# Kernel optimization log

Hardware: AMD Instinct MI355X
Metric: run time of the kernel (lower is better)

## Reference

```python
import jax, jax.numpy as jnp
import numpy as np

N, F, H, Z = 80, 64, 256, 128
OFF = N * (N - 1) // 2  # 3160
E = 800
MPM_ITERS = 50


def _gcn(x, src, dst, W, b, n):
    # PyG GCNConv: add self-loops, symmetric normalization D^-1/2 (A+I) D^-1/2, then +bias
    h = x @ W
    ones = jnp.ones(src.shape[0], dtype=h.dtype)
    deg = jax.ops.segment_sum(ones, dst, num_segments=n)
    dinv = jax.lax.rsqrt(jnp.maximum(deg, 1e-12))
    norm = dinv[src] * dinv[dst]
    out = jax.ops.segment_sum(h[src] * norm[:, None], dst, num_segments=n)
    return out + b


def _bn(h, g, b):
    # BatchNorm1d, training mode (biased batch stats), eps=1e-5
    m = h.mean(0)
    v = ((h - m) ** 2).mean(0)
    return g * (h - m) * jax.lax.rsqrt(v + 1e-5) + b


def setup_inputs() -> dict:
    key = jax.random.key(0)
    ks = jax.random.split(key, 32)
    rn = lambda k, s, sc=0.05: (jax.random.normal(k, s, dtype=jnp.float32) * sc)
    inp = {
        'x': jax.random.normal(ks[0], (N, F), dtype=jnp.float32),
        'edge_index': jax.random.randint(ks[1], (2, E), 0, N, dtype=jnp.int32),
        'adj': jax.random.randint(ks[2], (N, N), 0, 2, dtype=jnp.int32),
        'eps': jax.random.normal(ks[3], (1, Z), dtype=jnp.float32),
        'W1': rn(ks[4], (F, H)), 'b1': jnp.zeros((H,), jnp.float32),
        'g1': jnp.ones((H,), jnp.float32), 'bt1': jnp.zeros((H,), jnp.float32),
        'W2': rn(ks[5], (H, H)), 'b2': jnp.zeros((H,), jnp.float32),
        'g2': jnp.ones((H,), jnp.float32), 'bt2': jnp.zeros((H,), jnp.float32),
        'Wmu': rn(ks[6], (H, Z)), 'bmu': jnp.zeros((Z,), jnp.float32),
        'Wlv': rn(ks[7], (H, Z)), 'blv': jnp.zeros((Z,), jnp.float32),
        'We1': rn(ks[8], (Z, H)), 'be1': jnp.zeros((H,), jnp.float32),
        'We2': rn(ks[9], (H, OFF)), 'be2': jnp.zeros((OFF,), jnp.float32),
        'Wn1': rn(ks[10], (Z, H)), 'bn1': jnp.zeros((H,), jnp.float32),
        'Wn2': rn(ks[11], (H, N)), 'bn2': jnp.zeros((N,), jnp.float32),
    }
    return inp


def reference(x, edge_index, adj, eps, W1, b1, g1, bt1, W2, b2, g2, bt2,
              Wmu, bmu, Wlv, blv, We1, be1, We2, be2, Wn1, bn1, Wn2, bn2):
    n = N
    # ---- encoder: GCN -> BN -> ReLU (x2), mean pool over real nodes ----
    sl = jnp.arange(n, dtype=edge_index.dtype)
    src = jnp.concatenate([edge_index[0], sl])
    dst = jnp.concatenate([edge_index[1], sl])
    h = jax.nn.relu(_bn(_gcn(x, src, dst, W1, b1, n), g1, bt1))
    h = jax.nn.relu(_bn(_gcn(h, src, dst, W2, b2, n), g2, bt2))
    g_vec = h.sum(0, keepdims=True) / n  # [1,H], R_int == n
    mu = g_vec @ Wmu + bmu
    logvar = jnp.clip(g_vec @ Wlv + blv, -4.0, 4.0)
    z = mu + eps * jnp.exp(0.5 * logvar)  # reparam
    # ---- decoder ----
    vec_logits = (jax.nn.relu(z @ We1 + be1) @ We2 + be2)[0]   # [OFF]
    node_logits = (jax.nn.relu(z @ Wn1 + bn1) @ Wn2 + bn2)[0]  # [N]
    iu, ju = np.triu_indices(n, k=1)
    A_hat = jnp.zeros((n, n), jnp.float32).at[iu, ju].set(vec_logits)
    A_hat = A_hat + A_hat.T
    d = jnp.arange(n)
    A_hat = A_hat.at[d, d].set(node_logits)  # A_hat_logits
    # ---- edge similarity tensor S [N,N,N,N] ----
    A = jnp.maximum(adj, adj.T).astype(jnp.float32)
    A = A.at[d, d].set(1.0)
    B = jax.nn.sigmoid(A_hat).at[d, d].set(1.0)
    degA, degB = A.sum(1), B.sum(1)
    node_sim = 1.0 / (jnp.abs(degA[:, None] - degB[None, :]) + 1.0)
    dA, dB = jnp.diag(A), jnp.diag(B)  # all ones by construction (faithful to source)
    S = (A * dA[:, None] * dA[None, :])[:, :, None, None] * \
        (B * dB[:, None] * dB[None, :])[None, None, :, :]
    eye = jnp.eye(n, dtype=bool)
    xor = eye[:, :, None, None] ^ eye[None, None, :, :]
    S = jnp.where(xor, 0.0, S)
    both = eye[:, :, None, None] & eye[None, None, :, :]
    S = jnp.where(both, node_sim[:, None, :, None], S)
    # ---- MPM fixed point (fixed 50 iterations) ----
    notey = (~eye).astype(S.dtype)[:, :, None]  # [i,j,1]
    X0 = jnp.full((n, n), 1.0 / n, dtype=jnp.float32)

    def step(X, _):
        node_term = X * node_sim
        XS_max = jnp.max(S * X[None, :, None, :], axis=-1)  # [i,j,a] = max_b X[j,b]*S[i,j,a,b]
        edge_term = jnp.sum(XS_max * notey, axis=1)          # sum over j != i
        Xn = node_term + edge_term
        Xn = Xn / jnp.linalg.norm(Xn)
        return Xn, None

    X, _ = jax.lax.scan(step, X0, None, length=MPM_ITERS)
    return X
```

## Files before the change

kernel.cpp:

```cpp
#include <hip/hip_runtime.h>


#define NN 80
#define PBLK 20
#define TPB 320
#define RP 84
#define NCOLS 13

__device__ __forceinline__ void gbar(int* ctr, int target){
  __syncthreads();
  if (threadIdx.x == 0){
    __hip_atomic_fetch_add(ctr, 1, __ATOMIC_RELEASE, __HIP_MEMORY_SCOPE_AGENT);
    while (__hip_atomic_load(ctr, __ATOMIC_ACQUIRE, __HIP_MEMORY_SCOPE_AGENT) < target)
      __builtin_amdgcn_s_sleep(1);
  }
  __syncthreads();
}

__device__ __forceinline__ float wave_sum(float v){
  #pragma unroll
  for (int k = 32; k >= 1; k >>= 1) v += __shfl_xor(v, k, 64);
  return v;
}

__device__ void gcn_bn_relu(const float* inL, float* outT,
                            const float* bias, const float* gamma, const float* beta,
                            const int* ei, const float* dinv,
                            float* accL, float* colstat, int p, int tid)
{
  for (int u = tid; u < NCOLS*NN; u += TPB) accL[u] = 0.f;
  __syncthreads();
  for (int cl = 0; cl < NCOLS; cl++){
    int c = p + PBLK*cl; if (c >= 256) break;
    const float* col = &inL[cl*NN];
    for (int e = tid; e < 800; e += TPB){
      int sidx = ei[e], didx = ei[800+e];
      atomicAdd(&accL[cl*NN + didx], col[sidx]*dinv[sidx]*dinv[didx]);
    }
  }
  __syncthreads();
  for (int u = tid; u < NCOLS*NN; u += TPB){
    int cl = u/NN, i = u - cl*NN, c = p + PBLK*cl;
    if (c < 256) accL[u] += inL[cl*NN+i]*dinv[i]*dinv[i] + bias[c];
  }
  __syncthreads();
  if (tid < NCOLS){
    int c = p + PBLK*tid;
    if (c < 256){
      const float* a = &accL[tid*NN];
      float m = 0.f;
      for (int i = 0; i < NN; i++) m += a[i];
      m *= (1.0f/NN);
      float v = 0.f;
      for (int i = 0; i < NN; i++){ float d = a[i]-m; v += d*d; }
      v *= (1.0f/NN);
      colstat[2*tid]   = m;
      colstat[2*tid+1] = 1.0f/sqrtf(v + 1e-5f);
    }
  }
  __syncthreads();
  for (int u = tid; u < NCOLS*NN; u += TPB){
    int cl = u/NN, i = u - cl*NN, c = p + PBLK*cl;
    if (c < 256){
      float hv = gamma[c]*(accL[u]-colstat[2*cl])*colstat[2*cl+1] + beta[c];
      outT[c*NN+i] = fmaxf(hv, 0.f);
    }
  }
}

__global__ __launch_bounds__(TPB, 1) void gvae_fused(
    const float* __restrict__ x,  const int* __restrict__ ei, const int* __restrict__ adj,
    const float* __restrict__ eps,
    const float* __restrict__ W1, const float* __restrict__ b1, const float* __restrict__ g1, const float* __restrict__ bt1,
    const float* __restrict__ W2, const float* __restrict__ b2, const float* __restrict__ g2, const float* __restrict__ bt2,
    const float* __restrict__ Wmu,const float* __restrict__ bmu,const float* __restrict__ Wlv,const float* __restrict__ blv,
    const float* __restrict__ We1,const float* __restrict__ be1,const float* __restrict__ We2,const float* __restrict__ be2,
    float* __restrict__ out, float* __restrict__ ws)
{
  const int tid = threadIdx.x;
  const int p   = blockIdx.x;

  int*   ctr   = (int*)ws;
  float* sumsq = ws + 16;
  float* hT    = ws + 128;
  float* h2T   = hT  + 20480;
  float* Bm    = h2T + 20480;
  float* Xb0   = Bm  + 6400;
  float* Xb1   = Xb0 + 6400;

  __shared__ float Xs[NN*RP];
  __shared__ float MtL[4*RP];
  __shared__ float red[8];
  __shared__ float dinv[NN];
  __shared__ float accL[NCOLS*NN];
  __shared__ float hL[NCOLS*NN];
  __shared__ float gv[256], zv[128], t1v[256];
  __shared__ float colstat[2*NCOLS];

  for (int i = tid; i < NN; i += TPB) accL[i] = 1.0f;
  __syncthreads();
  for (int e = tid; e < 800; e += TPB) atomicAdd(&accL[ei[800+e]], 1.0f);
  __syncthreads();
  for (int i = tid; i < NN; i += TPB) dinv[i] = 1.0f/sqrtf(accL[i]);
  __syncthreads();

  for (int u = tid; u < NCOLS*NN; u += TPB){
    int cl = u/NN, i = u - cl*NN, c = p + PBLK*cl;
    if (c < 256){
      float s = 0.f;
      for (int k = 0; k < 64; k++) s += x[i*64+k]*W1[k*256+c];
      hL[u] = s;
    }
  }
  __syncthreads();
  gcn_bn_relu(hL, hT, b1, g1, bt1, ei, dinv, accL, colstat, p, tid);
  gbar(ctr, 1*PBLK);

  for (int u = tid; u < 20*NCOLS; u += TPB){
    int cl = u/20, iq = u - cl*20, c = p + PBLK*cl;
    if (c < 256){
      int i0 = 4*iq;
      float a0=0.f,a1=0.f,a2=0.f,a3=0.f;
      for (int k = 0; k < 256; k++){
        float wv = W2[k*256+c];
        float4 hv = *(const float4*)&hT[k*NN+i0];
        a0 += hv.x*wv; a1 += hv.y*wv; a2 += hv.z*wv; a3 += hv.w*wv;
      }
      hL[cl*NN+i0+0]=a0; hL[cl*NN+i0+1]=a1; hL[cl*NN+i0+2]=a2; hL[cl*NN+i0+3]=a3;
    }
  }
  __syncthreads();
  gcn_bn_relu(hL, h2T, b2, g2, bt2, ei, dinv, accL, colstat, p, tid);
  gbar(ctr, 2*PBLK);

  for (int c = tid; c < 256; c += TPB){
    const float* r = &h2T[c*NN];
    float s = 0.f;
    for (int i = 0; i < NN; i++) s += r[i];
    gv[c] = s*(1.0f/NN);
  }
  __syncthreads();
  for (int c = tid; c < 128; c += TPB){
    float smu = bmu[c], slv = blv[c];
    for (int k = 0; k < 256; k++){
      float g = gv[k];
      smu += g*Wmu[k*128+c];
      slv += g*Wlv[k*128+c];
    }
    slv = fminf(fmaxf(slv, -4.f), 4.f);
    zv[c] = smu + eps[c]*expf(0.5f*slv);
  }
  __syncthreads();
  for (int c = tid; c < 256; c += TPB){
    float s = be1[c];
    for (int k = 0; k < 128; k++) s += zv[k]*We1[k*256+c];
    t1v[c] = fmaxf(s, 0.f);
  }
  __syncthreads();
  for (int r = 0; r < 4; r++){
    int i = p + PBLK*r;
    if (tid == 0) Bm[i*NN+i] = 1.0f;
    for (int j = i+1+tid; j < NN; j += TPB){
      int off = i*(2*NN-1-i)/2 + (j-i-1);
      float s = be2[off];
      for (int k = 0; k < 256; k++) s += t1v[k]*We2[k*3160+off];
      float sg = 1.0f/(1.0f + expf(-s));
      Bm[i*NN+j] = sg;
      Bm[j*NN+i] = sg;
    }
  }
  gbar(ctr, 3*PBLK);

  const int w  = tid >> 6;
  const int l  = tid & 63;
  const int il = 16*w + (l & 15);
  const int ae = l >> 4;
  const int al = 4*p + ae;

  float4 Af[20], Bf[20];
  float degA = 0.f, degB = 0.f;
  #pragma unroll
  for (int c = 0; c < 20; c++){
    int j0 = 4*c;
    int4 ar = *(const int4*)&adj[il*NN+j0];
    int q0 = adj[(j0+0)*NN+il];
    int q1 = adj[(j0+1)*NN+il];
    int q2 = adj[(j0+2)*NN+il];
    int q3 = adj[(j0+3)*NN+il];
    float4 a;
    a.x = ((ar.x|q0) != 0 || il == j0+0) ? 1.f : 0.f;
    a.y = ((ar.y|q1) != 0 || il == j0+1) ? 1.f : 0.f;
    a.z = ((ar.z|q2) != 0 || il == j0+2) ? 1.f : 0.f;
    a.w = ((ar.w|q3) != 0 || il == j0+3) ? 1.f : 0.f;
    Af[c] = a;
    degA += (a.x+a.y)+(a.z+a.w);
  }
  #pragma unroll
  for (int c = 0; c < 20; c++){
    float4 b = *(const float4*)&Bm[al*NN+4*c];
    Bf[c] = b;
    degB += (b.x+b.y)+(b.z+b.w);
  }
  const float ns = 1.0f/(fabsf(degA-degB)+1.0f);
  #pragma unroll
  for (int c = 0; c < 20; c++){
    if (c == p){
      if      (ae == 0) Bf[c].x = 0.f;
      else if (ae == 1) Bf[c].y = 0.f;
      else if (ae == 2) Bf[c].z = 0.f;
      else              Bf[c].w = 0.f;
    }
  }

  for (int u = tid; u < NN*RP; u += TPB) Xs[u] = 1.0f/NN;
  float xn = 0.f;
  int bar = 3;
  for (int t = 0; t < 50; t++){
    if (t > 0){
      const float* Xsrc = ((t-1)&1) ? Xb1 : Xb0;
      for (int u = tid; u < NN*20; u += TPB){
        int j = u/20, c4 = (u - j*20)*4;
        *(float4*)&Xs[j*RP+c4] = *(const float4*)&Xsrc[j*NN+c4];
      }
    }
    __syncthreads();
    float sc = 1.0f;
    if (t > 0)
      sc = 1.0f/sqrtf(__hip_atomic_load(&sumsq[t], __ATOMIC_RELAXED, __HIP_MEMORY_SCOPE_AGENT));

    float m = 0.f;
    #pragma unroll
    for (int c = 0; c < 20; c++){
      float4 xv = *(const float4*)&Xs[il*RP+4*c];
      float p0 = xv.x*Bf[c].x, p1 = xv.y*Bf[c].y, p2 = xv.z*Bf[c].z, p3 = xv.w*Bf[c].w;
      m = fmaxf(m, fmaxf(fmaxf(p0,p1), fmaxf(p2,p3)));
    }
    float xnode = Xs[il*RP+al];
    MtL[ae*RP+il] = m;
    __syncthreads();

    float e0=0.f,e1=0.f,e2=0.f,e3=0.f;
    #pragma unroll
    for (int c = 0; c < 20; c++){
      float4 mv = *(const float4*)&MtL[ae*RP+4*c];
      e0 += Af[c].x*mv.x; e1 += Af[c].y*mv.y; e2 += Af[c].z*mv.z; e3 += Af[c].w*mv.w;
    }
    float edge = ((e0+e1)+(e2+e3)) - m;
    xn = sc*(ns*xnode + edge);

    if (t < 49){
      float* Xdst = (t&1) ? Xb1 : Xb0;
      Xdst[il*NN+al] = xn;
    }
    float v = wave_sum(xn*xn);
    if (l == 0) red[w] = v;
    __syncthreads();
    if (tid == 0){
      float tot = ((red[0]+red[1])+(red[2]+red[3]))+red[4];
      __hip_atomic_fetch_add(&sumsq[t+1], tot, __ATOMIC_RELAXED, __HIP_MEMORY_SCOPE_AGENT);
    }
    bar++;
    gbar(ctr, bar*PBLK);
  }
  float sf = 1.0f/sqrtf(__hip_atomic_load(&sumsq[50], __ATOMIC_RELAXED, __HIP_MEMORY_SCOPE_AGENT));
  out[il*NN+al] = xn*sf;
}

extern "C" void kernel_launch(void* const* d_in, const int* in_sizes, int n_in,
                              void* d_out, int out_size, void* d_ws, size_t ws_size,
                              hipStream_t stream)
{
  (void)in_sizes; (void)n_in; (void)out_size; (void)ws_size;
  hipMemsetAsync(d_ws, 0, 512, stream);
  gvae_fused<<<PBLK, TPB, 0, stream>>>(
      (const float*)d_in[0],  (const int*)d_in[1],   (const int*)d_in[2],   (const float*)d_in[3],
      (const float*)d_in[4],  (const float*)d_in[5],  (const float*)d_in[6],  (const float*)d_in[7],
      (const float*)d_in[8],  (const float*)d_in[9],  (const float*)d_in[10], (const float*)d_in[11],
      (const float*)d_in[12], (const float*)d_in[13], (const float*)d_in[14], (const float*)d_in[15],
      (const float*)d_in[16], (const float*)d_in[17], (const float*)d_in[18], (const float*)d_in[19],
      (float*)d_out, (float*)d_ws);
}
```

Baseline: 509.4 us.

## Replace per-iteration grid barrier with per-block flag publish of norm partials

Each MPM iteration no longer uses an atomic-counter grid barrier plus an atomic sum. Instead every block publishes its partial sum of squares into a per-iteration flag slot, and one wave spins until all 20 slots are non-zero, then reduces them locally. X values are written and read with relaxed agent-scope atomics, and a vmcnt wait orders the data stores before the flag. The norm is now computed right after the barrier-equivalent, and the 1/norm scale is applied to the final output. This removes the serialized counter atomics and the fence round-trips on the 50-iteration critical path. The risks are relying on partials being non-zero as a readiness signal and weaker memory ordering, since relaxed loads are used without an acquire.

```diff
diff --git a/kernel.cpp b/kernel.cpp
--- a/kernel.cpp
+++ b/kernel.cpp
@@ -6,13 +6,15 @@
 #define TPB 320
 #define RP 84
 #define NCOLS 13
+#define AGT __HIP_MEMORY_SCOPE_AGENT
 
 __device__ __forceinline__ void gbar(int* ctr, int target){
   __syncthreads();
   if (threadIdx.x == 0){
-    __hip_atomic_fetch_add(ctr, 1, __ATOMIC_RELEASE, __HIP_MEMORY_SCOPE_AGENT);
-    while (__hip_atomic_load(ctr, __ATOMIC_ACQUIRE, __HIP_MEMORY_SCOPE_AGENT) < target)
+    __hip_atomic_fetch_add(ctr, 1, __ATOMIC_RELEASE, AGT);
+    while (__hip_atomic_load(ctr, __ATOMIC_RELAXED, AGT) < target)
       __builtin_amdgcn_s_sleep(1);
+    (void)__hip_atomic_load(ctr, __ATOMIC_ACQUIRE, AGT);
   }
   __syncthreads();
 }
@@ -81,8 +83,8 @@
   const int p   = blockIdx.x;
 
   int*   ctr   = (int*)ws;
-  float* sumsq = ws + 16;
-  float* hT    = ws + 128;
+  float* flags = ws + 32;
+  float* hT    = ws + 2048;
   float* h2T   = hT  + 20480;
   float* Bm    = h2T + 20480;
   float* Xb0   = Bm  + 6400;
@@ -214,19 +216,9 @@
 
   for (int u = tid; u < NN*RP; u += TPB) Xs[u] = 1.0f/NN;
   float xn = 0.f;
-  int bar = 3;
+  float sc = 1.0f;
   for (int t = 0; t < 50; t++){
-    if (t > 0){
-      const float* Xsrc = ((t-1)&1) ? Xb1 : Xb0;
-      for (int u = tid; u < NN*20; u += TPB){
-        int j = u/20, c4 = (u - j*20)*4;
-        *(float4*)&Xs[j*RP+c4] = *(const float4*)&Xsrc[j*NN+c4];
-      }
-    }
-    __syncthreads();
-    float sc = 1.0f;
-    if (t > 0)
-      sc = 1.0f/sqrtf(__hip_atomic_load(&sumsq[t], __ATOMIC_RELAXED, __HIP_MEMORY_SCOPE_AGENT));
+    __syncthreads();
 
     float m = 0.f;
     #pragma unroll
@@ -250,20 +242,39 @@
 
     if (t < 49){
       float* Xdst = (t&1) ? Xb1 : Xb0;
-      Xdst[il*NN+al] = xn;
+      __hip_atomic_store(&Xdst[il*NN+al], xn, __ATOMIC_RELAXED, AGT);
     }
     float v = wave_sum(xn*xn);
     if (l == 0) red[w] = v;
     __syncthreads();
-    if (tid == 0){
-      float tot = ((red[0]+red[1])+(red[2]+red[3]))+red[4];
-      __hip_atomic_fetch_add(&sumsq[t+1], tot, __ATOMIC_RELAXED, __HIP_MEMORY_SCOPE_AGENT);
-    }
-    bar++;
-    gbar(ctr, bar*PBLK);
-  }
-  float sf = 1.0f/sqrtf(__hip_atomic_load(&sumsq[50], __ATOMIC_RELAXED, __HIP_MEMORY_SCOPE_AGENT));
-  out[il*NN+al] = xn*sf;
+
+    if (w == 0){
+      float part = ((red[0]+red[1])+(red[2]+red[3]))+red[4];
+      if (l == 0){
+        asm volatile("s_waitcnt vmcnt(0)" ::: "memory");
+        __hip_atomic_store(&flags[t*32+p], part, __ATOMIC_RELAXED, AGT);
+      }
+      float fv = 0.f;
+      for (;;){
+        if (l < 20 && fv == 0.f)
+          fv = __hip_atomic_load(&flags[t*32+l], __ATOMIC_RELAXED, AGT);
+        if (__all((l >= 20) || (fv != 0.f))) break;
+      }
+      float tot = wave_sum((l < 20) ? fv : 0.f);
+      if (l == 0) red[5] = tot;
+    }
+    __syncthreads();
+    sc = 1.0f/sqrtf(red[5]);
+
+    if (t < 49){
+      const float* Xsrc = (t&1) ? Xb1 : Xb0;
+      for (int u = tid; u < NN*NN; u += TPB){
+        int j = u/NN, c = u - j*NN;
+        Xs[j*RP+c] = __hip_atomic_load((float*)&Xsrc[u], __ATOMIC_RELAXED, AGT);
+      }
+    }
+  }
+  out[il*NN+al] = xn*sc;
 }
 
 extern "C" void kernel_launch(void* const* d_in, const int* in_sizes, int n_in,
@@ -271,7 +282,7 @@
                               hipStream_t stream)
 {
   (void)in_sizes; (void)n_in; (void)out_size; (void)ws_size;
-  hipMemsetAsync(d_ws, 0, 512, stream);
+  hipMemsetAsync(d_ws, 0, 8192, stream);
   gvae_fused<<<PBLK, TPB, 0, stream>>>(
       (const float*)d_in[0],  (const int*)d_in[1],   (const int*)d_in[2],   (const float*)d_in[3],
       (const float*)d_in[4],  (const float*)d_in[5],  (const float*)d_in[6],  (const float*)d_in[7],
```

New measurement: 653.1 us. 28.2% more time.

## Replace persistent grid barriers with per-stage and per-iteration kernel launches

Applied to the files above, without the earlier changes.

The single persistent kernel, which relied on atomic spin-wait grid barriers, is split into separate kernels: two encoder layers, the latent/decoder stage, an adjacency/degree prep stage, one launch per MPM iteration, and a final normalization kernel. Kernel boundaries now provide the cross-block synchronization. Per-block partial sums of squares are written to distinct slots and reduced by each consumer, so no atomics or memset are needed. The cost is about 55 launches, and each iteration reloads A/B rows from global memory instead of keeping them in registers.

```diff
diff --git a/kernel.cpp b/kernel.cpp
--- a/kernel.cpp
+++ b/kernel.cpp
@@ -7,15 +7,17 @@
 #define RP 84
 #define NCOLS 13
 
-__device__ __forceinline__ void gbar(int* ctr, int target){
-  __syncthreads();
-  if (threadIdx.x == 0){
-    __hip_atomic_fetch_add(ctr, 1, __ATOMIC_RELEASE, __HIP_MEMORY_SCOPE_AGENT);
-    while (__hip_atomic_load(ctr, __ATOMIC_ACQUIRE, __HIP_MEMORY_SCOPE_AGENT) < target)
-      __builtin_amdgcn_s_sleep(1);
-  }
-  __syncthreads();
-}
+typedef float f4 __attribute__((ext_vector_type(4)));
+
+#define WS_FLAGS 64
+#define WS_XB0   2048
+#define WS_XB1   8448
+#define WS_HT    14848
+#define WS_H2T   35328
+#define WS_BM    55808
+#define WS_AW    62208
+#define WS_DEGA  68608
+#define WS_DEGB  68688
 
 __device__ __forceinline__ float wave_sum(float v){
   #pragma unroll
@@ -68,42 +70,29 @@
   }
 }
 
-__global__ __launch_bounds__(TPB, 1) void gvae_fused(
-    const float* __restrict__ x,  const int* __restrict__ ei, const int* __restrict__ adj,
-    const float* __restrict__ eps,
-    const float* __restrict__ W1, const float* __restrict__ b1, const float* __restrict__ g1, const float* __restrict__ bt1,
-    const float* __restrict__ W2, const float* __restrict__ b2, const float* __restrict__ g2, const float* __restrict__ bt2,
-    const float* __restrict__ Wmu,const float* __restrict__ bmu,const float* __restrict__ Wlv,const float* __restrict__ blv,
-    const float* __restrict__ We1,const float* __restrict__ be1,const float* __restrict__ We2,const float* __restrict__ be2,
-    float* __restrict__ out, float* __restrict__ ws)
-{
-  const int tid = threadIdx.x;
-  const int p   = blockIdx.x;
-
-  int*   ctr   = (int*)ws;
-  float* sumsq = ws + 16;
-  float* hT    = ws + 128;
-  float* h2T   = hT  + 20480;
-  float* Bm    = h2T + 20480;
-  float* Xb0   = Bm  + 6400;
-  float* Xb1   = Xb0 + 6400;
-
-  __shared__ float Xs[NN*RP];
-  __shared__ float MtL[4*RP];
-  __shared__ float red[8];
+__device__ void mk_dinv(const int* ei, float* accL, float* dinv, int tid){
+  for (int i = tid; i < NN; i += TPB) accL[i] = 1.0f;
+  __syncthreads();
+  for (int e = tid; e < 800; e += TPB) atomicAdd(&accL[ei[800+e]], 1.0f);
+  __syncthreads();
+  for (int i = tid; i < NN; i += TPB) dinv[i] = 1.0f/sqrtf(accL[i]);
+  __syncthreads();
+}
+
+__global__ __launch_bounds__(TPB, 1) void enc1(
+    const float* __restrict__ x, const int* __restrict__ ei,
+    const float* __restrict__ W1, const float* __restrict__ b1,
+    const float* __restrict__ g1, const float* __restrict__ bt1,
+    float* __restrict__ ws)
+{
+  const int tid = threadIdx.x, p = blockIdx.x;
+  float* hT = ws + WS_HT;
   __shared__ float dinv[NN];
   __shared__ float accL[NCOLS*NN];
   __shared__ float hL[NCOLS*NN];
-  __shared__ float gv[256], zv[128], t1v[256];
   __shared__ float colstat[2*NCOLS];
 
-  for (int i = tid; i < NN; i += TPB) accL[i] = 1.0f;
-  __syncthreads();
-  for (int e = tid; e < 800; e += TPB) atomicAdd(&accL[ei[800+e]], 1.0f);
-  __syncthreads();
-  for (int i = tid; i < NN; i += TPB) dinv[i] = 1.0f/sqrtf(accL[i]);
-  __syncthreads();
-
+  mk_dinv(ei, accL, dinv, tid);
   for (int u = tid; u < NCOLS*NN; u += TPB){
     int cl = u/NN, i = u - cl*NN, c = p + PBLK*cl;
     if (c < 256){
@@ -114,8 +103,23 @@
   }
   __syncthreads();
   gcn_bn_relu(hL, hT, b1, g1, bt1, ei, dinv, accL, colstat, p, tid);
-  gbar(ctr, 1*PBLK);
-
+}
+
+__global__ __launch_bounds__(TPB, 1) void enc2(
+    const int* __restrict__ ei,
+    const float* __restrict__ W2, const float* __restrict__ b2,
+    const float* __restrict__ g2, const float* __restrict__ bt2,
+    float* __restrict__ ws)
+{
+  const int tid = threadIdx.x, p = blockIdx.x;
+  const float* hT = ws + WS_HT;
+  float* h2T = ws + WS_H2T;
+  __shared__ float dinv[NN];
+  __shared__ float accL[NCOLS*NN];
+  __shared__ float hL[NCOLS*NN];
+  __shared__ float colstat[2*NCOLS];
+
+  mk_dinv(ei, accL, dinv, tid);
   for (int u = tid; u < 20*NCOLS; u += TPB){
     int cl = u/20, iq = u - cl*20, c = p + PBLK*cl;
     if (c < 256){
@@ -131,7 +135,20 @@
   }
   __syncthreads();
   gcn_bn_relu(hL, h2T, b2, g2, bt2, ei, dinv, accL, colstat, p, tid);
-  gbar(ctr, 2*PBLK);
+}
+
+__global__ __launch_bounds__(TPB, 1) void enc3(
+    const float* __restrict__ eps,
+    const float* __restrict__ Wmu, const float* __restrict__ bmu,
+    const float* __restrict__ Wlv, const float* __restrict__ blv,
+    const float* __restrict__ We1, const float* __restrict__ be1,
+    const float* __restrict__ We2, const float* __restrict__ be2,
+    float* __restrict__ ws)
+{
+  const int tid = threadIdx.x, p = blockIdx.x;
+  const float* h2T = ws + WS_H2T;
+  float* Bm = ws + WS_BM;
+  __shared__ float gv[256], zv[128], t1v[256];
 
   for (int c = tid; c < 256; c += TPB){
     const float* r = &h2T[c*NN];
@@ -169,7 +186,55 @@
       Bm[j*NN+i] = sg;
     }
   }
-  gbar(ctr, 3*PBLK);
+}
+
+__global__ __launch_bounds__(TPB, 1) void prep(
+    const int* __restrict__ adj, float* __restrict__ ws)
+{
+  const int tid = threadIdx.x, p = blockIdx.x;
+  const float* Bm = ws + WS_BM;
+  float* Aw = ws + WS_AW;
+  float* degA = ws + WS_DEGA;
+  float* degB = ws + WS_DEGB;
+  __shared__ float AwL[4*NN];
+
+  int r = tid/NN, j = tid - r*NN, row = 4*p + r;
+  float v = (((adj[row*NN+j] | adj[j*NN+row]) != 0) || (row == j)) ? 1.f : 0.f;
+  AwL[r*NN+j] = v;
+  Aw[row*NN+j] = v;
+  __syncthreads();
+  if (tid < 4){
+    const float4* ar = (const float4*)&AwL[tid*NN];
+    float dg = 0.f;
+    #pragma unroll
+    for (int c = 0; c < 20; c++){
+      float4 a = ar[c];
+      dg += (a.x+a.y)+(a.z+a.w);
+    }
+    degA[4*p+tid] = dg;
+  } else if (tid < 8){
+    int a0 = 4*p + (tid-4);
+    const float4* br = (const float4*)&Bm[a0*NN];
+    float dg = 0.f;
+    #pragma unroll
+    for (int c = 0; c < 20; c++){
+      float4 b = br[c];
+      dg += (b.x+b.y)+(b.z+b.w);
+    }
+    degB[a0] = dg;
+  }
+}
+
+__global__ __launch_bounds__(TPB, 1) void mpm_step(int t, float* __restrict__ ws)
+{
+  const int tid = threadIdx.x, p = blockIdx.x;
+  float* flags = ws + WS_FLAGS;
+  float* Xb0   = ws + WS_XB0;
+  float* Xb1   = ws + WS_XB1;
+  const float* Bm   = ws + WS_BM;
+  const float* Aw   = ws + WS_AW;
+  const float* degA = ws + WS_DEGA;
+  const float* degB = ws + WS_DEGB;
 
   const int w  = tid >> 6;
   const int l  = tid & 63;
@@ -177,93 +242,90 @@
   const int ae = l >> 4;
   const int al = 4*p + ae;
 
-  float4 Af[20], Bf[20];
-  float degA = 0.f, degB = 0.f;
+  __shared__ float Xs[NN*RP];
+  __shared__ float MtL[4*RP];
+  __shared__ float red[8];
+
+  f4 Bf[20], Af[20];
+  const f4* brow = (const f4*)&Bm[al*NN];
+  const f4* arow = (const f4*)&Aw[il*NN];
+  #pragma unroll
+  for (int c = 0; c < 20; c++){ Bf[c] = brow[c]; Af[c] = arow[c]; }
+  {
+    int dc = al >> 2, de = al & 3;
+    if      (de == 0) Bf[dc].x = 0.f;
+    else if (de == 1) Bf[dc].y = 0.f;
+    else if (de == 2) Bf[dc].z = 0.f;
+    else              Bf[dc].w = 0.f;
+  }
+  const float ns = 1.0f/(fabsf(degA[il]-degB[al])+1.0f);
+
+  float sc = 1.0f;
+  if (t > 0){
+    float fv = (l < PBLK) ? flags[(t-1)*32 + l] : 0.f;
+    sc = 1.0f/sqrtf(wave_sum(fv));
+  }
+
+  if (t == 0){
+    for (int u = tid; u < NN*RP; u += TPB) Xs[u] = 1.0f/NN;
+  } else {
+    const f4* S4 = (const f4*)(((t-1)&1) ? Xb1 : Xb0);
+    #pragma unroll
+    for (int c5 = 0; c5 < 5; c5++){
+      int q = tid + TPB*c5;
+      f4 v4 = S4[q];
+      int i = q/20, a0 = 4*(q - 20*i);
+      *(f4*)&Xs[i*RP + a0] = v4;
+    }
+  }
+  __syncthreads();
+
+  float m = 0.f;
   #pragma unroll
   for (int c = 0; c < 20; c++){
-    int j0 = 4*c;
-    int4 ar = *(const int4*)&adj[il*NN+j0];
-    int q0 = adj[(j0+0)*NN+il];
-    int q1 = adj[(j0+1)*NN+il];
-    int q2 = adj[(j0+2)*NN+il];
-    int q3 = adj[(j0+3)*NN+il];
-    float4 a;
-    a.x = ((ar.x|q0) != 0 || il == j0+0) ? 1.f : 0.f;
-    a.y = ((ar.y|q1) != 0 || il == j0+1) ? 1.f : 0.f;
-    a.z = ((ar.z|q2) != 0 || il == j0+2) ? 1.f : 0.f;
-    a.w = ((ar.w|q3) != 0 || il == j0+3) ? 1.f : 0.f;
-    Af[c] = a;
-    degA += (a.x+a.y)+(a.z+a.w);
-  }
+    float4 xv = *(const float4*)&Xs[il*RP+4*c];
+    float p0 = xv.x*Bf[c].x, p1 = xv.y*Bf[c].y, p2 = xv.z*Bf[c].z, p3 = xv.w*Bf[c].w;
+    m = fmaxf(m, fmaxf(fmaxf(p0,p1), fmaxf(p2,p3)));
+  }
+  float xnode = Xs[il*RP+al];
+  MtL[ae*RP+il] = m;
+  __syncthreads();
+
+  float e0=0.f,e1=0.f,e2=0.f,e3=0.f;
   #pragma unroll
   for (int c = 0; c < 20; c++){
-    float4 b = *(const float4*)&Bm[al*NN+4*c];
-    Bf[c] = b;
-    degB += (b.x+b.y)+(b.z+b.w);
-  }
-  const float ns = 1.0f/(fabsf(degA-degB)+1.0f);
-  #pragma unroll
-  for (int c = 0; c < 20; c++){
-    if (c == p){
-      if      (ae == 0) Bf[c].x = 0.f;
-      else if (ae == 1) Bf[c].y = 0.f;
-      else if (ae == 2) Bf[c].z = 0.f;
-      else              Bf[c].w = 0.f;
-    }
-  }
-
-  for (int u = tid; u < NN*RP; u += TPB) Xs[u] = 1.0f/NN;
-  float xn = 0.f;
-  int bar = 3;
-  for (int t = 0; t < 50; t++){
-    if (t > 0){
-      const float* Xsrc = ((t-1)&1) ? Xb1 : Xb0;
-      for (int u = tid; u < NN*20; u += TPB){
-        int j = u/20, c4 = (u - j*20)*4;
-        *(float4*)&Xs[j*RP+c4] = *(const float4*)&Xsrc[j*NN+c4];
-      }
-    }
-    __syncthreads();
-    float sc = 1.0f;
-    if (t > 0)
-      sc = 1.0f/sqrtf(__hip_atomic_load(&sumsq[t], __ATOMIC_RELAXED, __HIP_MEMORY_SCOPE_AGENT));
-
-    float m = 0.f;
-    #pragma unroll
-    for (int c = 0; c < 20; c++){
-      float4 xv = *(const float4*)&Xs[il*RP+4*c];
-      float p0 = xv.x*Bf[c].x, p1 = xv.y*Bf[c].y, p2 = xv.z*Bf[c].z, p3 = xv.w*Bf[c].w;
-      m = fmaxf(m, fmaxf(fmaxf(p0,p1), fmaxf(p2,p3)));
-    }
-    float xnode = Xs[il*RP+al];
-    MtL[ae*RP+il] = m;
-    __syncthreads();
-
-    float e0=0.f,e1=0.f,e2=0.f,e3=0.f;
-    #pragma unroll
-    for (int c = 0; c < 20; c++){
-      float4 mv = *(const float4*)&MtL[ae*RP+4*c];
-      e0 += Af[c].x*mv.x; e1 += Af[c].y*mv.y; e2 += Af[c].z*mv.z; e3 += Af[c].w*mv.w;
-    }
-    float edge = ((e0+e1)+(e2+e3)) - m;
-    xn = sc*(ns*xnode + edge);
-
-    if (t < 49){
-      float* Xdst = (t&1) ? Xb1 : Xb0;
-      Xdst[il*NN+al] = xn;
-    }
-    float v = wave_sum(xn*xn);
-    if (l == 0) red[w] = v;
-    __syncthreads();
-    if (tid == 0){
-      float tot = ((red[0]+red[1])+(red[2]+red[3]))+red[4];
-      __hip_atomic_fetch_add(&sumsq[t+1], tot, __ATOMIC_RELAXED, __HIP_MEMORY_SCOPE_AGENT);
-    }
-    bar++;
-    gbar(ctr, bar*PBLK);
-  }
-  float sf = 1.0f/sqrtf(__hip_atomic_load(&sumsq[50], __ATOMIC_RELAXED, __HIP_MEMORY_SCOPE_AGENT));
-  out[il*NN+al] = xn*sf;
+    float4 mv = *(const float4*)&MtL[ae*RP+4*c];
+    e0 += Af[c].x*mv.x; e1 += Af[c].y*mv.y; e2 += Af[c].z*mv.z; e3 += Af[c].w*mv.w;
+  }
+  float edge = ((e0+e1)+(e2+e3)) - m;
+  float xn = sc*(ns*xnode + edge);
+
+  float* Xdst = (t&1) ? Xb1 : Xb0;
+  Xdst[il*NN+al] = xn;
+
+  float v = wave_sum(xn*xn);
+  if (l == 0) red[w] = v;
+  __syncthreads();
+  if (tid == 0){
+    float part = ((red[0]+red[1])+(red[2]+red[3]))+red[4];
+    flags[t*32+p] = part;
+  }
+}
+
+__global__ __launch_bounds__(TPB, 1) void fin(
+    const float* __restrict__ ws, float* __restrict__ out)
+{
+  const int tid = threadIdx.x, p = blockIdx.x;
+  const float* flags = ws + WS_FLAGS;
+  const float* X49   = ws + WS_XB1;
+  const int w  = tid >> 6;
+  const int l  = tid & 63;
+  const int il = 16*w + (l & 15);
+  const int ae = l >> 4;
+  const int al = 4*p + ae;
+  float fv = (l < PBLK) ? flags[49*32 + l] : 0.f;
+  float scf = 1.0f/sqrtf(wave_sum(fv));
+  out[il*NN+al] = X49[il*NN+al]*scf;
 }
 
 extern "C" void kernel_launch(void* const* d_in, const int* in_sizes, int n_in,
@@ -271,12 +333,23 @@
                               hipStream_t stream)
 {
   (void)in_sizes; (void)n_in; (void)out_size; (void)ws_size;
-  hipMemsetAsync(d_ws, 0, 512, stream);
-  gvae_fused<<<PBLK, TPB, 0, stream>>>(
-      (const float*)d_in[0],  (const int*)d_in[1],   (const int*)d_in[2],   (const float*)d_in[3],
-      (const float*)d_in[4],  (const float*)d_in[5],  (const float*)d_in[6],  (const float*)d_in[7],
-      (const float*)d_in[8],  (const float*)d_in[9],  (const float*)d_in[10], (const float*)d_in[11],
-      (const float*)d_in[12], (const float*)d_in[13], (const float*)d_in[14], (const float*)d_in[15],
-      (const float*)d_in[16], (const float*)d_in[17], (const float*)d_in[18], (const float*)d_in[19],
-      (float*)d_out, (float*)d_ws);
-}
+  float* ws = (float*)d_ws;
+  enc1<<<PBLK, TPB, 0, stream>>>(
+      (const float*)d_in[0], (const int*)d_in[1],
+      (const float*)d_in[4], (const float*)d_in[5],
+      (const float*)d_in[6], (const float*)d_in[7], ws);
+  enc2<<<PBLK, TPB, 0, stream>>>(
+      (const int*)d_in[1],
+      (const float*)d_in[8], (const float*)d_in[9],
+      (const float*)d_in[10], (const float*)d_in[11], ws);
+  enc3<<<PBLK, TPB, 0, stream>>>(
+      (const float*)d_in[3],
+      (const float*)d_in[12], (const float*)d_in[13],
+      (const float*)d_in[14], (const float*)d_in[15],
+      (const float*)d_in[16], (const float*)d_in[17],
+      (const float*)d_in[18], (const float*)d_in[19], ws);
+  prep<<<PBLK, TPB, 0, stream>>>((const int*)d_in[2], ws);
+  for (int t = 0; t < 50; t++)
+    mpm_step<<<PBLK, TPB, 0, stream>>>(t, ws);
+  fin<<<PBLK, TPB, 0, stream>>>(ws, (float*)d_out);
+}
```

Measured after the change: 827.8 us. 1.62x slower.
